# Kernel tuning notes

Measured on AMD Instinct MI355X. Metric: run time of the kernel, lower is better.

The kernel has to match this reference:

```python
import jax, jax.numpy as jnp
import numpy as np

# Irreps config: input/output = 32x0e + 16x1o (dim 80), H=4 heads -> head = 8x0e + 4x1o (dim 20)
M0, M1 = 32, 16      # input muls for 0e / 1o
m0, m1 = 8, 4        # per-head muls
H = 4
HEAD_DIM = m0 + 3 * m1   # 20
WNUM = H * (M0 * m0 + M1 * m0 + M0 * m1 + M1 * m1)  # 2304 per-edge TP weights
NB, HID = 16, 64
SQRT3 = np.float32(np.sqrt(3.0))
EPS = 1e-8


def radial_mlp(x, W1, b1, W2, b2):
    return jax.nn.silu(x @ W1 + b1) @ W2 + b2


def tp_edge(ss, vv, sh0, sh1, w):
    """FullyConnectedTensorProduct (32x0e+16x1o) x (1x0e+1x1o) -> H*(8x0e+4x1o) with per-edge weights w [E, WNUM].
    Paths: 0e*0e->0e, 1o*1o->0e (CG dot/sqrt3), 0e*1o->1o, 1o*0e->1o; path norm 1/sqrt(fan_in)."""
    E = ss.shape[0]
    per = M0 * m0 + M1 * m0 + M0 * m1 + M1 * m1  # 576
    w = w.reshape(E, H, per)
    o = 0
    Wss = w[..., o:o + M0 * m0].reshape(E, H, M0, m0); o += M0 * m0
    Wvv = w[..., o:o + M1 * m0].reshape(E, H, M1, m0); o += M1 * m0
    Wsv = w[..., o:o + M0 * m1].reshape(E, H, M0, m1); o += M0 * m1
    Wvs = w[..., o:o + M1 * m1].reshape(E, H, M1, m1)
    fan = np.float32(np.sqrt(M0 + M1))  # fan_in = 48 for both output irreps
    vv_dot = jnp.einsum('eui,ei->eu', vv, sh1) / SQRT3
    out0 = (jnp.einsum('eu,ehuw->ehw', ss * sh0[:, None], Wss)
            + jnp.einsum('eu,ehuw->ehw', vv_dot, Wvv)) / fan          # [E,H,m0]
    out1 = (jnp.einsum('eu,ehuw->ehw', ss, Wsv)[..., None] * sh1[:, None, None, :]
            + jnp.einsum('eui,ehuw->ehwi', vv * sh0[:, None, None], Wvs)) / fan  # [E,H,m1,3]
    return out0, out1


def setup_inputs() -> dict:
    key = jax.random.key(0)
    ks = jax.random.split(key, 24)
    N, E = 2000, 32000
    g = lambda k, s, sc=1.0: jax.random.normal(k, s, jnp.float32) * sc
    inp = {}
    inp['node_features'] = g(ks[0], (N, M0 + 3 * M1))
    inp['edge_index'] = jax.random.randint(ks[1], (2, E), 0, N)
    inp['edge_sh'] = g(ks[2], (E, 4))
    inp['edge_radial_emb'] = jax.random.uniform(ks[3], (E, NB), jnp.float32)
    # query e3nn Linear (per-head blocks)
    inp['Wq0'] = g(ks[4], (H, M0, m0))
    inp['Wq1'] = g(ks[5], (H, M1, m1))
    # radial MLPs for key / value TP weights
    inp['Wk1'] = g(ks[6], (NB, HID), 1 / np.sqrt(NB)); inp['bk1'] = jnp.zeros((HID,), jnp.float32)
    inp['Wk2'] = g(ks[7], (HID, WNUM), 1 / np.sqrt(HID)); inp['bk2'] = jnp.zeros((WNUM,), jnp.float32)
    inp['Wv1'] = g(ks[8], (NB, HID), 1 / np.sqrt(NB)); inp['bv1'] = jnp.zeros((HID,), jnp.float32)
    inp['Wv2'] = g(ks[9], (HID, WNUM), 1 / np.sqrt(HID)); inp['bv2'] = jnp.zeros((WNUM,), jnp.float32)
    # single-head dot-product TP -> 0e (shared weights)
    inp['Wd0'] = g(ks[10], (m0, m0))
    inp['Wd1'] = g(ks[11], (m1, m1))
    # output projection Linear (all heads mixed per irrep)
    inp['Wo0'] = g(ks[12], (H * m0, M0))
    inp['Wo1'] = g(ks[13], (H * m1, M1))
    # FFN: out irreps -> (2*M0)x0e + M1x1o -> out irreps
    inp['Wf1_0'] = g(ks[14], (M0, 2 * M0))
    inp['Wf1_1'] = g(ks[15], (M1, M1))
    inp['Wf2_0'] = g(ks[16], (2 * M0, M0))
    inp['Wf2_1'] = g(ks[17], (M1, M1))
    return inp


def reference(node_features, edge_index, edge_sh, edge_radial_emb,
              Wq0, Wq1, Wk1, bk1, Wk2, bk2, Wv1, bv1, Wv2, bv2,
              Wd0, Wd1, Wo0, Wo1, Wf1_0, Wf1_1, Wf2_0, Wf2_1):
    N = node_features.shape[0]
    s = node_features[:, :M0]                       # [N, M0] scalars
    v = node_features[:, M0:].reshape(N, M1, 3)     # [N, M1, 3] vectors
    src, dst = edge_index[0], edge_index[1]

    # query Linear (e3nn: per-irrep channel mix, norm 1/sqrt(fan_in))
    q0 = jnp.einsum('nu,huw->nhw', s, Wq0) / np.sqrt(M0)
    q1 = jnp.einsum('nui,huw->nhwi', v, Wq1) / np.sqrt(M1)

    sh0, sh1 = edge_sh[:, 0], edge_sh[:, 1:4]
    ss, vv = s[src], v[src]                         # gather per edge

    wk = radial_mlp(edge_radial_emb, Wk1, bk1, Wk2, bk2)
    wv = radial_mlp(edge_radial_emb, Wv1, bv1, Wv2, bv2)
    k0, k1 = tp_edge(ss, vv, sh0, sh1, wk)
    v0, v1 = tp_edge(ss, vv, sh0, sh1, wv)

    # per-head equivariant dot product -> 0e logits
    qd0, qd1 = q0[dst], q1[dst]
    fan_d = np.float32(np.sqrt(m0 * m0 + m1 * m1))
    logits = (jnp.einsum('ehu,uv,ehv->eh', qd0, Wd0, k0)
              + jnp.einsum('ehui,uv,ehvi->eh', qd1, Wd1, k1) / SQRT3) / fan_d
    logits = logits / np.sqrt(HEAD_DIM)             # self.scale
    logits = jnp.clip(logits, -10.0, 10.0)

    # scatter softmax over edges sharing a destination node
    seg_max = jax.ops.segment_max(logits, dst, num_segments=N)
    seg_max = jnp.maximum(seg_max, -10.0)           # handle empty segments
    ex = jnp.exp(logits - seg_max[dst])
    denom = jax.ops.segment_sum(ex, dst, num_segments=N)
    alpha = ex / (denom[dst] + 1e-12)               # [E, H]

    agg0 = jax.ops.segment_sum(alpha[..., None] * v0, dst, num_segments=N)        # [N,H,m0]
    agg1 = jax.ops.segment_sum(alpha[..., None, None] * v1, dst, num_segments=N)  # [N,H,m1,3]

    # output projection Linear over concatenated heads
    o0 = agg0.reshape(N, H * m0) @ Wo0 / np.sqrt(H * m0)
    o1 = jnp.einsum('nui,uw->nwi', agg1.reshape(N, H * m1, 3), Wo1) / np.sqrt(H * m1)

    # residual (input irreps == output irreps -> identity skip)
    x0 = s + o0
    x1 = v + o1

    # FFN with SafeNormActivation
    f0 = x0 @ Wf1_0 / np.sqrt(M0)                               # [N, 2*M0]
    f1 = jnp.einsum('nui,uw->nwi', x1, Wf1_1) / np.sqrt(M1)     # [N, M1, 3]
    a0 = jax.nn.silu(f0)
    norms = jnp.linalg.norm(f1, axis=-1, keepdims=True)
    safe = jnp.maximum(norms, EPS)
    a1 = jnp.where(norms < EPS, 0.0, (f1 / safe) * jax.nn.silu(norms))
    g0 = a0 @ Wf2_0 / np.sqrt(2 * M0)
    g1 = jnp.einsum('nui,uw->nwi', a1, Wf2_1) / np.sqrt(M1)

    out0 = x0 + g0
    out1 = x1 + g1
    return jnp.concatenate([out0, out1.reshape(N, M1 * 3)], axis=-1)
```

## Files before the change

### kernel.cpp

```cpp
#include <hip/hip_runtime.h>

typedef unsigned int uint;
typedef unsigned short ushort;
typedef __attribute__((ext_vector_type(8))) short bf16x8;
typedef __attribute__((ext_vector_type(4))) float f32x4;
typedef __attribute__((ext_vector_type(2))) float f32x2;

#define N_NODES 2000
#define N_EDGES 32000
#define WNUM 2304

constexpr size_t OFF_AGG0 = 0;
constexpr size_t OFF_AGG1 = 64000;
constexpr size_t OFF_DEN  = 160000;
constexpr size_t OFF_FLAG = 170000;
constexpr size_t OFF_W2T  = 170004;
constexpr size_t OFF_QT0  = 317460;
constexpr size_t OFF_QT1  = 381460;
constexpr size_t OFF_W1T  = 509460;
constexpr size_t OFF_W1P  = 511508;

__device__ __forceinline__ float b2f(ushort u){ union{uint i; float f;}x; x.i=((uint)u)<<16; return x.f; }
__device__ __forceinline__ float lo16(uint w){ union{uint u; float f;}x; x.u=w<<16; return x.f; }
__device__ __forceinline__ float hi16(uint w){ union{uint u; float f;}x; x.u=w&0xFFFF0000u; return x.f; }
__device__ __forceinline__ ushort f2b(float f){
  union{float f; uint u;}x; x.f=f;
  uint r = (x.u + 0x7FFFu + ((x.u>>16)&1u)) >> 16;
  return (ushort)r;
}
__device__ __forceinline__ float siluf(float x){ return x / (1.f + __expf(-x)); }

template<bool F32>
__device__ __forceinline__ float ldf(const void* p, int i){
  if (F32) return ((const float*)p)[i];
  return b2f(((const ushort*)p)[i]);
}
__device__ __forceinline__ float ldfr(const void* p, int i, bool f32){
  return f32 ? ((const float*)p)[i] : b2f(((const ushort*)p)[i]);
}

template<bool F32>
__device__ void prep_body(
    const void* __restrict__ nf,
    const void* __restrict__ Wk2, const void* __restrict__ Wv2,
    const void* __restrict__ Wk1, const void* __restrict__ Wv1,
    const void* __restrict__ Wq0, const void* __restrict__ Wq1,
    const void* __restrict__ Wd0, const void* __restrict__ Wd1,
    ushort* __restrict__ W2T, float* __restrict__ W1T, uint* __restrict__ W1P,
    float* __restrict__ qt0, float* __restrict__ qt1,
    float* __restrict__ aggz){
  const int t = threadIdx.x;
  const int bid = blockIdx.x;

  if (bid < 72){
    __shared__ ushort tile[64][66];
    const int mat = bid / 36, jt = bid - mat*36;
    const void* W = mat ? Wv2 : Wk2;
    const int j0 = jt*64;
    const int jo = t & 63, cb = t >> 6;
    #pragma unroll
    for (int k=0; k<16; ++k){
      const int c = cb + k*4;
      tile[c][jo] = F32 ? f2b(((const float*)W)[(size_t)c*WNUM + j0 + jo])
                        : ((const ushort*)W)[(size_t)c*WNUM + j0 + jo];
    }
    __syncthreads();
    const int jl = t >> 2, c0 = (t & 3)*16;
    ushort* dst = W2T + (size_t)mat*147456 + (size_t)(j0+jl)*64 + c0;
    #pragma unroll
    for (int k=0; k<16; ++k) dst[k] = tile[c0+k][jl];
  } else if (bid < 104){
    __shared__ float nfL[64][80];
    __shared__ float wq0L[1024], wq1L[256], wd0L[64], wd1L[16];
    const int nb = bid - 72, n0 = nb*64;
    if (F32){
      for (int idx=t; idx<1280; idx+=256){
        const int gi = n0*20 + idx;
        float4 v;
        if (gi < 40000) v = ((const float4*)nf)[gi];
        else { v.x=0.f; v.y=0.f; v.z=0.f; v.w=0.f; }
        ((float4*)&nfL[0][0])[idx] = v;
      }
    } else {
      for (int idx=t; idx<640; idx+=256){
        const int gi = n0*10 + idx;
        uint4 v;
        if (gi < 20000) v = ((const uint4*)nf)[gi];
        else { v.x=0u; v.y=0u; v.z=0u; v.w=0u; }
        float* d = &nfL[0][0] + idx*8;
        d[0]=lo16(v.x); d[1]=hi16(v.x); d[2]=lo16(v.y); d[3]=hi16(v.y);
        d[4]=lo16(v.z); d[5]=hi16(v.z); d[6]=lo16(v.w); d[7]=hi16(v.w);
      }
    }
    for (int idx=t; idx<1024; idx+=256) wq0L[idx] = ldf<F32>(Wq0, idx);
    if (t < 256) wq1L[t] = ldf<F32>(Wq1, t);
    if (t < 64)  wd0L[t] = ldf<F32>(Wd0, t);
    if (t < 16)  wd1L[t] = ldf<F32>(Wd1, t);
    __syncthreads();
    const int nl = t >> 2, h = t & 3;
    const int nn = n0 + nl;
    if (nn < N_NODES){
      const float* S = &nfL[nl][0];
      float q0[8];
      #pragma unroll
      for (int w=0; w<8; ++w){
        float a = 0.f;
        #pragma unroll
        for (int u=0; u<32; ++u) a += S[u]*wq0L[h*256 + u*8 + w];
        q0[w] = a * 0.17677669529663687f;
      }
      #pragma unroll
      for (int vv=0; vv<8; ++vv){
        float a = 0.f;
        #pragma unroll
        for (int u=0; u<8; ++u) a += q0[u]*wd0L[u*8+vv];
        qt0[nn*32 + h*8 + vv] = a;
      }
      float q1[12];
      #pragma unroll
      for (int w=0; w<4; ++w)
        #pragma unroll
        for (int i=0; i<3; ++i){
          float a = 0.f;
          #pragma unroll
          for (int u=0; u<16; ++u) a += S[32+u*3+i]*wq1L[h*64 + u*4 + w];
          q1[w*3+i] = a * 0.25f;
        }
      #pragma unroll
      for (int vv=0; vv<4; ++vv)
        #pragma unroll
        for (int i=0; i<3; ++i){
          float a = 0.f;
          #pragma unroll
          for (int u=0; u<4; ++u) a += q1[u*3+i]*wd1L[u*4+vv];
          qt1[nn*48 + h*12 + vv*3 + i] = a;
        }
    }
  } else if (bid == 104){
    for (int idx=t; idx<2048; idx+=256){
      const int mat = idx >> 10, rem = idx & 1023;
      const int c = rem >> 4, b = rem & 15;
      W1T[idx] = ldf<F32>(mat ? Wv1 : Wk1, b*64 + c);
    }
    for (int idx=t; idx<1024; idx+=256){
      const int mat = idx >> 9, rem = idx & 511;
      const int c = rem >> 3, j = rem & 7;
      const void* W = mat ? Wv1 : Wk1;
      ushort u0, u1;
      if (F32){ u0 = f2b(((const float*)W)[(2*j)*64+c]); u1 = f2b(((const float*)W)[(2*j+1)*64+c]); }
      else    { u0 = ((const ushort*)W)[(2*j)*64+c];     u1 = ((const ushort*)W)[(2*j+1)*64+c]; }
      W1P[idx] = (uint)u0 | ((uint)u1 << 16);
    }
  } else {
    float4 z; z.x=0.f; z.y=0.f; z.z=0.f; z.w=0.f;
    for (int i = (bid-105)*256 + t; i < 42000; i += 4096)
      ((float4*)aggz)[i] = z;
  }
}

__global__ __launch_bounds__(256) void prep_kernel(
    const void* nf,
    const void* Wk2, const void* Wv2,
    const void* Wk1, const void* Wv1,
    const void* Wq0, const void* Wq1,
    const void* Wd0, const void* Wd1,
    ushort* W2T, float* W1T, uint* W1P, float* qt0, float* qt1,
    float* aggz, int* flag){
  __shared__ int s_cnt;
  const int t = threadIdx.x;
  if (t == 0) s_cnt = 0;
  __syncthreads();
  {
    uint u = ((const ushort*)nf)[t*2];
    uint ex = (u >> 7) & 0xFFu;
    if (ex >= 0xA0u) atomicAdd(&s_cnt, 1);
  }
  __syncthreads();
  const bool F32 = (s_cnt >= 20);
  if (blockIdx.x == 0 && t == 0) *flag = F32 ? 1 : 0;
  if (F32) prep_body<true >(nf, Wk2, Wv2, Wk1, Wv1, Wq0, Wq1, Wd0, Wd1, W2T, W1T, W1P, qt0, qt1, aggz);
  else     prep_body<false>(nf, Wk2, Wv2, Wk1, Wv1, Wq0, Wq1, Wd0, Wd1, W2T, W1T, W1P, qt0, qt1, aggz);
}

struct Smem {
  ushort hidA[8192];
  union {
    struct {
      float fssT[32][66];
      float fvvT[16][66];
      float sslT[32][66];
    } f;
    float cont[5376];
  } u;
  float vshT[3][16][66];
  float sh1T[3][66];
  float park0[2][4][64][8];
  float parkP[2][4][64][4];
  float exL[64][4];
  int   dstL[64];
};

__device__ __forceinline__ f32x4 mma_pair(const bf16x8& a0f, const bf16x8& a1f,
                                          bf16x8 b0, bf16x8 b1, float bb){
  f32x4 c = {bb,bb,bb,bb};
  c = __builtin_amdgcn_mfma_f32_16x16x32_bf16(a0f, b0, c, 0,0,0);
  c = __builtin_amdgcn_mfma_f32_16x16x32_bf16(a1f, b1, c, 0,0,0);
  return c;
}
__device__ __forceinline__ void acc_feat(const f32x4 c, const float* fp, float* acc){
  f32x2 fA = *(const f32x2*)(fp);
  f32x2 fB = *(const f32x2*)(fp + 2);
  acc[0] += c[0]*fA[0]; acc[1] += c[1]*fA[1];
  acc[2] += c[2]*fB[0]; acc[3] += c[3]*fB[1];
}

template<bool F32>
__device__ void edge_body(
    const void* __restrict__ nf,  const int* __restrict__ eidx,
    const void* __restrict__ esh, const void* __restrict__ emb,
    const float* __restrict__ W1T, const uint* __restrict__ W1P,
    const void* __restrict__ bk1, const void* __restrict__ bk2,
    const void* __restrict__ bv1, const void* __restrict__ bv2,
    const ushort* __restrict__ W2T,
    const float* __restrict__ qt0g, const float* __restrict__ qt1g,
    float* __restrict__ agg0, float* __restrict__ agg1, float* __restrict__ denom,
    Smem& sm){
  const int t  = threadIdx.x;
  const int geb = blockIdx.x*64;

  {
    const int g = t >> 5, r = t & 31;
    int geA[4], srcA[4], dstA[4];
    float shv0[4], shv1[4], shv2[4], shv3[4];
    #pragma unroll
    for (int e=0; e<4; ++e) geA[e] = geb + g*4 + e;
    #pragma unroll
    for (int e=0; e<4; ++e){ srcA[e] = eidx[geA[e]]; dstA[e] = eidx[N_EDGES + geA[e]]; }
    #pragma unroll
    for (int e=0; e<4; ++e){
      if (F32){
        float4 s4 = ((const float4*)esh)[geA[e]];
        shv0[e]=s4.x; shv1[e]=s4.y; shv2[e]=s4.z; shv3[e]=s4.w;
      } else {
        uint2 u2 = ((const uint2*)esh)[geA[e]];
        shv0[e]=lo16(u2.x); shv1[e]=hi16(u2.x); shv2[e]=lo16(u2.y); shv3[e]=hi16(u2.y);
      }
    }
    #pragma unroll
    for (int e=0; e<4; ++e){
      const int le = g*4+e, src = srcA[e];
      const float sh0 = shv0[e], s1a = shv1[e], s1b = shv2[e], s1c = shv3[e];
      if (r == 0) sm.dstL[le] = dstA[e];
      if (r < 3) sm.sh1T[r][le] = (r==0)? s1a : (r==1)? s1b : s1c;
      float sv = ldf<F32>(nf, src*80 + r);
      sm.u.f.sslT[r][le] = sv;
      sm.u.f.fssT[r][le] = sv * sh0;
      if (r < 16){
        float v0 = ldf<F32>(nf, src*80+32+r*3+0);
        float v1 = ldf<F32>(nf, src*80+32+r*3+1);
        float v2 = ldf<F32>(nf, src*80+32+r*3+2);
        sm.vshT[0][r][le] = v0*sh0; sm.vshT[1][r][le] = v1*sh0; sm.vshT[2][r][le] = v2*sh0;
        sm.u.f.fvvT[r][le] = (v0*s1a + v1*s1b + v2*s1c) * 0.5773502691896258f;
      }
    }
  }

  {
    const int c  = t & 63;
    const int g8 = t >> 6;
    const int le0 = g8*8;
    float bkv = ldf<F32>(bk1, c), bvv = ldf<F32>(bv1, c);
    f32x4 wkF[4], wvF[4];
    uint4 wkB[2], wvB[2];
    if (F32){
      const f32x4* pk = (const f32x4*)(W1T + c*16);
      const f32x4* pv = (const f32x4*)(W1T + 1024 + c*16);
      wkF[0]=pk[0]; wkF[1]=pk[1]; wkF[2]=pk[2]; wkF[3]=pk[3];
      wvF[0]=pv[0]; wvF[1]=pv[1]; wvF[2]=pv[2]; wvF[3]=pv[3];
    } else {
      const uint4* pk = (const uint4*)(W1P + c*8);
      const uint4* pv = (const uint4*)(W1P + 512 + c*8);
      wkB[0]=pk[0]; wkB[1]=pk[1];
      wvB[0]=pv[0]; wvB[1]=pv[1];
    }
    uint4 ra, rb; float4 fa, fb, fc, fd;
    if (F32){
      const float4* p = (const float4*)emb + (size_t)(geb+le0)*4;
      fa = p[0]; fb = p[1]; fc = p[2]; fd = p[3];
    } else {
      const uint4* p = (const uint4*)emb + (size_t)(geb+le0)*2;
      ra = p[0]; rb = p[1];
    }
    #pragma unroll
    for (int e=0; e<8; ++e){
      float em[16];
      if (F32){
        em[0]=fa.x; em[1]=fa.y; em[2]=fa.z; em[3]=fa.w;
        em[4]=fb.x; em[5]=fb.y; em[6]=fb.z; em[7]=fb.w;
        em[8]=fc.x; em[9]=fc.y; em[10]=fc.z; em[11]=fc.w;
        em[12]=fd.x; em[13]=fd.y; em[14]=fd.z; em[15]=fd.w;
      } else {
        em[0]=lo16(ra.x); em[1]=hi16(ra.x); em[2]=lo16(ra.y); em[3]=hi16(ra.y);
        em[4]=lo16(ra.z); em[5]=hi16(ra.z); em[6]=lo16(ra.w); em[7]=hi16(ra.w);
        em[8]=lo16(rb.x); em[9]=hi16(rb.x); em[10]=lo16(rb.y); em[11]=hi16(rb.y);
        em[12]=lo16(rb.z); em[13]=hi16(rb.z); em[14]=lo16(rb.w); em[15]=hi16(rb.w);
      }
      if (e < 7){
        if (F32){
          const float4* p = (const float4*)emb + (size_t)(geb+le0+e+1)*4;
          fa = p[0]; fb = p[1]; fc = p[2]; fd = p[3];
        } else {
          const uint4* p = (const uint4*)emb + (size_t)(geb+le0+e+1)*2;
          ra = p[0]; rb = p[1];
        }
      }
      const int le = le0+e;
      float ak = bkv, av = bvv;
      if (F32){
        #pragma unroll
        for (int g=0; g<4; ++g)
          #pragma unroll
          for (int j=0; j<4; ++j){
            ak += em[g*4+j]*wkF[g][j];
            av += em[g*4+j]*wvF[g][j];
          }
      } else {
        #pragma unroll
        for (int g=0; g<2; ++g){
          const uint4 a = wkB[g], b = wvB[g];
          ak += em[g*8+0]*lo16(a.x) + em[g*8+1]*hi16(a.x)
              + em[g*8+2]*lo16(a.y) + em[g*8+3]*hi16(a.y)
              + em[g*8+4]*lo16(a.z) + em[g*8+5]*hi16(a.z)
              + em[g*8+6]*lo16(a.w) + em[g*8+7]*hi16(a.w);
          av += em[g*8+0]*lo16(b.x) + em[g*8+1]*hi16(b.x)
              + em[g*8+2]*lo16(b.y) + em[g*8+3]*hi16(b.y)
              + em[g*8+4]*lo16(b.z) + em[g*8+5]*hi16(b.z)
              + em[g*8+6]*lo16(b.w) + em[g*8+7]*hi16(b.w);
        }
      }
      const int idx = (le>>4)*1024 + (c>>5)*512 + ((((c>>3)&3)*16 + (le&15))<<3) + (c&7);
      sm.hidA[idx]        = f2b(siluf(ak));
      sm.hidA[4096 + idx] = f2b(siluf(av));
    }
  }
  __syncthreads();

  const int w  = t >> 6;
  const int kv = w >> 2;
  const int h  = w & 3;
  const int lane = t & 63, q = lane >> 4, n = lane & 15;
  const float invfan = 0.14433756729740643f;

  const ushort* wptr = W2T + (size_t)kv*147456 + h*36864 + n*64 + q*8;
  const void* bvec = kv ? bv2 : bk2;
  const int bi0 = h*576 + n;
  const float* fb_ss = &sm.u.f.fssT[n>>3][q*4];
  const float* fb_sl = &sm.u.f.sslT[n>>2][q*4];
  const int nq2 = n>>2;

  bf16x8 af[4][2];
  #pragma unroll
  for (int Mt=0; Mt<4; ++Mt)
    #pragma unroll
    for (int kh=0; kh<2; ++kh)
      af[Mt][kh] = *(const bf16x8*)&sm.hidA[kv*4096 + Mt*1024 + kh*512 + lane*8];

#define PREF(P0,P1,PB,TL) \
  P0 = *(const bf16x8*)(wptr + (TL)*1024); \
  P1 = *(const bf16x8*)(wptr + (TL)*1024 + 32); \
  PB = ldf<F32>(bvec, bi0 + (TL)*16);

  bf16x8 pA0, pA1, pB0, pB1; float pAb, pBb;
  PREF(pA0, pA1, pAb, 0);
  PREF(pB0, pB1, pBb, 1);

  {
    float a0[4][4];
    #pragma unroll
    for (int Mt=0; Mt<4; ++Mt){ a0[Mt][0]=0.f; a0[Mt][1]=0.f; a0[Mt][2]=0.f; a0[Mt][3]=0.f; }
    #pragma unroll 2
    for (int tl=0; tl<24; tl+=2){
      { bf16x8 b0=pA0, b1=pA1; float bb=pAb;
        PREF(pA0, pA1, pAb, tl+2);
        const float* fp = fb_ss + tl*132;
        #pragma unroll
        for (int Mt=0; Mt<4; ++Mt) acc_feat(mma_pair(af[Mt][0], af[Mt][1], b0, b1, bb), fp + Mt*16, a0[Mt]); }
      { bf16x8 b0=pB0, b1=pB1; float bb=pBb;
        PREF(pB0, pB1, pBb, tl+3);
        const float* fp = fb_ss + (tl+1)*132;
        #pragma unroll
        for (int Mt=0; Mt<4; ++Mt) acc_feat(mma_pair(af[Mt][0], af[Mt][1], b0, b1, bb), fp + Mt*16, a0[Mt]); }
    }
    #pragma unroll
    for (int Mt=0; Mt<4; ++Mt)
      #pragma unroll
      for (int z=0; z<4; ++z){
        a0[Mt][z] += __shfl_xor(a0[Mt][z], 8, 64);
        if (n < 8) sm.park0[kv][h][Mt*16 + q*4 + z][n] = a0[Mt][z];
      }
  }

  {
    float aP[4][4];
    #pragma unroll
    for (int Mt=0; Mt<4; ++Mt){ aP[Mt][0]=0.f; aP[Mt][1]=0.f; aP[Mt][2]=0.f; aP[Mt][3]=0.f; }
    #pragma unroll 2
    for (int tl=24; tl<32; tl+=2){
      { bf16x8 b0=pA0, b1=pA1; float bb=pAb;
        PREF(pA0, pA1, pAb, tl+2);
        const float* fp = fb_sl + (tl-24)*264;
        #pragma unroll
        for (int Mt=0; Mt<4; ++Mt) acc_feat(mma_pair(af[Mt][0], af[Mt][1], b0, b1, bb), fp + Mt*16, aP[Mt]); }
      { bf16x8 b0=pB0, b1=pB1; float bb=pBb;
        PREF(pB0, pB1, pBb, tl+3);
        const float* fp = fb_sl + (tl-23)*264;
        #pragma unroll
        for (int Mt=0; Mt<4; ++Mt) acc_feat(mma_pair(af[Mt][0], af[Mt][1], b0, b1, bb), fp + Mt*16, aP[Mt]); }
    }
    #pragma unroll
    for (int Mt=0; Mt<4; ++Mt)
      #pragma unroll
      for (int z=0; z<4; ++z){
        aP[Mt][z] += __shfl_xor(aP[Mt][z], 4, 64);
        aP[Mt][z] += __shfl_xor(aP[Mt][z], 8, 64);
        if (n < 4) sm.parkP[kv][h][Mt*16 + q*4 + z][n] = aP[Mt][z];
      }
  }

  float aW[3][4][4];
  #pragma unroll
  for (int i=0; i<3; ++i)
    #pragma unroll
    for (int Mt=0; Mt<4; ++Mt){ aW[i][Mt][0]=0.f; aW[i][Mt][1]=0.f; aW[i][Mt][2]=0.f; aW[i][Mt][3]=0.f; }
#define BODY_AW(B0,B1,BB,TL) { \
    const int u = ((TL)-32)*4 + nq2; \
    _Pragma("unroll") \
    for (int Mt=0; Mt<4; ++Mt){ \
      f32x4 c = mma_pair(af[Mt][0], af[Mt][1], B0, B1, BB); \
      _Pragma("unroll") \
      for (int i=0; i<3; ++i) acc_feat(c, &sm.vshT[i][u][Mt*16+q*4], aW[i][Mt]); \
    } }
  { bf16x8 b0=pA0, b1=pA1; float bb=pAb; PREF(pA0, pA1, pAb, 34); BODY_AW(b0,b1,bb,32); }
  { bf16x8 b0=pB0, b1=pB1; float bb=pBb; PREF(pB0, pB1, pBb, 35); BODY_AW(b0,b1,bb,33); }
  { bf16x8 b0=pA0, b1=pA1; float bb=pAb; BODY_AW(b0,b1,bb,34); }
  { bf16x8 b0=pB0, b1=pB1; float bb=pBb; BODY_AW(b0,b1,bb,35); }
#undef BODY_AW
#undef PREF
  #pragma unroll
  for (int i=0; i<3; ++i)
    #pragma unroll
    for (int Mt=0; Mt<4; ++Mt)
      #pragma unroll
      for (int z=0; z<4; ++z){
        aW[i][Mt][z] += __shfl_xor(aW[i][Mt][z], 4, 64);
        aW[i][Mt][z] += __shfl_xor(aW[i][Mt][z], 8, 64);
      }

  if (kv == 0){
    float lgp[4][4];
    #pragma unroll
    for (int Mt=0; Mt<4; ++Mt)
      #pragma unroll
      for (int z=0; z<4; ++z){
        const int el = Mt*16 + q*4 + z;
        const int d = sm.dstL[el];
        float acc = 0.f;
        if (n < 8) acc = qt0g[d*32 + h*8 + n] * sm.park0[0][h][el][n];
        if (n < 4){
          const float aPv = sm.parkP[0][h][el][n];
          float s = 0.f;
          #pragma unroll
          for (int i=0; i<3; ++i){
            float k1 = aPv*sm.sh1T[i][el] + aW[i][Mt][z];
            s += qt1g[d*48 + h*12 + n*3 + i] * k1;
          }
          acc += s * 0.5773502691896258f;
        }
        lgp[Mt][z] = acc;
      }
    #pragma unroll
    for (int Mt=0; Mt<4; ++Mt)
      #pragma unroll
      for (int z=0; z<4; ++z){
        lgp[Mt][z] += __shfl_xor(lgp[Mt][z], 1, 64);
        lgp[Mt][z] += __shfl_xor(lgp[Mt][z], 2, 64);
        lgp[Mt][z] += __shfl_xor(lgp[Mt][z], 4, 64);
        lgp[Mt][z] += __shfl_xor(lgp[Mt][z], 8, 64);
      }
    if (n == 0){
      #pragma unroll
      for (int Mt=0; Mt<4; ++Mt)
        #pragma unroll
        for (int z=0; z<4; ++z){
          float lg = lgp[Mt][z] * invfan * 0.025f;
          lg = fminf(10.f, fmaxf(-10.f, lg));
          sm.exL[Mt*16 + q*4 + z][h] = __expf(lg - 10.0f);
        }
    }
  }
  __syncthreads();

  if (kv == 1){
    #pragma unroll
    for (int Mt=0; Mt<4; ++Mt)
      #pragma unroll
      for (int z=0; z<4; ++z){
        const int el = Mt*16 + q*4 + z;
        const float ex = sm.exL[el][h];
        float* cp = &sm.u.cont[el*84 + h*21];
        if (n == 0) cp[0] = ex;
        if (n < 8)  cp[1+n] = ex * sm.park0[1][h][el][n] * invfan;
        if (n < 4){
          const float aPv = sm.parkP[1][h][el][n];
          #pragma unroll
          for (int i=0; i<3; ++i){
            float v1 = (aPv*sm.sh1T[i][el] + aW[i][Mt][z]) * invfan;
            cp[9+n*3+i] = ex * v1;
          }
        }
      }
  }
  __syncthreads();

  #pragma unroll
  for (int k=0; k<11; ++k){
    const int idx = t + k*512;
    if (idx < 5376){
      const int el = idx / 84;
      const int cm = idx - el*84;
      const int h2 = cm / 21;
      const int comp = cm - h2*21;
      const float val = sm.u.cont[idx];
      const int d2 = sm.dstL[el];
      if (comp == 0)      atomicAdd(denom + d2*4  + h2, val);
      else if (comp < 9)  atomicAdd(agg0  + d2*32 + h2*8  + (comp-1), val);
      else                atomicAdd(agg1  + d2*48 + h2*12 + (comp-9), val);
    }
  }
}

__global__ __launch_bounds__(512) void edge_kernel(
    const void* nf, const int* eidx, const void* esh, const void* emb,
    const float* W1T, const uint* W1P,
    const void* bk1, const void* bk2,
    const void* bv1, const void* bv2,
    const ushort* W2T, const float* qt0g, const float* qt1g,
    float* agg0, float* agg1, float* denom, const int* flag){
  __shared__ Smem sm;
  if (*flag)
    edge_body<true >(nf,eidx,esh,emb,W1T,W1P,bk1,bk2,bv1,bv2,W2T,qt0g,qt1g,agg0,agg1,denom,sm);
  else
    edge_body<false>(nf,eidx,esh,emb,W1T,W1P,bk1,bk2,bv1,bv2,W2T,qt0g,qt1g,agg0,agg1,denom,sm);
}

__global__ __launch_bounds__(256) void node_out_kernel(
    const void* __restrict__ nf, const float* __restrict__ agg0r, const float* __restrict__ agg1r,
    const float* __restrict__ denom,
    const void* __restrict__ Wo0, const void* __restrict__ Wo1,
    const void* __restrict__ Wf10, const void* __restrict__ Wf11,
    const void* __restrict__ Wf20, const void* __restrict__ Wf21,
    void* __restrict__ out, const int* __restrict__ flag){
  __shared__ float ag0[4][32], ag1[4][48], adiv[4][4];
  __shared__ float x0s[4][32], x1s[4][48], a0s[4][64], f1s[4][48], coefs[4][16];
  const bool F32 = (*flag) != 0;
  const int s = threadIdx.x >> 6, t = threadIdx.x & 63;
  const int n = blockIdx.x*4 + s;
  if (t < 4) adiv[s][t] = 1.f / (denom[n*4+t] + 1e-12f);
  __syncthreads();
  if (t < 32) ag0[s][t] = agg0r[n*32+t] * adiv[s][t>>3];
  if (t < 48) ag1[s][t] = agg1r[n*48+t] * adiv[s][t/12];
  __syncthreads();
  if (t < 32){
    float o = 0.f;
    #pragma unroll
    for (int k=0; k<32; ++k) o += ag0[s][k]*ldfr(Wo0, k*32+t, F32);
    x0s[s][t] = ldfr(nf, n*80+t, F32) + o*0.17677669529663687f;
  }
  if (t < 48){
    int w = t/3, i = t - w*3;
    float o = 0.f;
    #pragma unroll
    for (int u=0; u<16; ++u) o += ag1[s][u*3+i]*ldfr(Wo1, u*16+w, F32);
    x1s[s][t] = ldfr(nf, n*80+32+t, F32) + o*0.25f;
  }
  __syncthreads();
  {
    float f0 = 0.f;
    #pragma unroll
    for (int u=0; u<32; ++u) f0 += x0s[s][u]*ldfr(Wf10, u*64+t, F32);
    a0s[s][t] = siluf(f0*0.17677669529663687f);
  }
  if (t < 48){
    int w = t/3, i = t - w*3;
    float f1 = 0.f;
    #pragma unroll
    for (int u=0; u<16; ++u) f1 += x1s[s][u*3+i]*ldfr(Wf11, u*16+w, F32);
    f1s[s][t] = f1*0.25f;
  }
  __syncthreads();
  if (t < 16){
    float a = f1s[s][t*3], b = f1s[s][t*3+1], c = f1s[s][t*3+2];
    float nrm = sqrtf(a*a+b*b+c*c);
    float safe = fmaxf(nrm, 1e-8f);
    coefs[s][t] = (nrm < 1e-8f) ? 0.f : siluf(nrm)/safe;
  }
  __syncthreads();
  if (t < 32){
    float g = 0.f;
    #pragma unroll
    for (int u=0; u<64; ++u) g += a0s[s][u]*ldfr(Wf20, u*32+t, F32);
    float val = x0s[s][t] + g*0.125f;
    if (F32) ((float*)out)[n*80+t] = val; else ((ushort*)out)[n*80+t] = f2b(val);
  }
  if (t < 48){
    int w = t/3, i = t - w*3;
    float g = 0.f;
    #pragma unroll
    for (int u=0; u<16; ++u) g += coefs[s][u]*f1s[s][u*3+i]*ldfr(Wf21, u*16+w, F32);
    float val = x1s[s][t] + g*0.25f;
    if (F32) ((float*)out)[n*80+32+t] = val; else ((ushort*)out)[n*80+32+t] = f2b(val);
  }
}

extern "C" void kernel_launch(void* const* d_in, const int* in_sizes, int n_in,
                              void* d_out, int out_size, void* d_ws, size_t ws_size,
                              hipStream_t stream){
  const void* nf   = d_in[0];
  const int*  eidx = (const int*)d_in[1];
  const void* esh  = d_in[2];
  const void* emb  = d_in[3];
  const void* Wq0  = d_in[4];
  const void* Wq1  = d_in[5];
  const void* Wk1  = d_in[6];
  const void* bk1  = d_in[7];
  const void* Wk2  = d_in[8];
  const void* bk2  = d_in[9];
  const void* Wv1  = d_in[10];
  const void* bv1  = d_in[11];
  const void* Wv2  = d_in[12];
  const void* bv2  = d_in[13];
  const void* Wd0  = d_in[14];
  const void* Wd1  = d_in[15];
  const void* Wo0  = d_in[16];
  const void* Wo1  = d_in[17];
  const void* Wf10 = d_in[18];
  const void* Wf11 = d_in[19];
  const void* Wf20 = d_in[20];
  const void* Wf21 = d_in[21];
  float* ws = (float*)d_ws;

  float* agg0  = ws + OFF_AGG0;
  float* agg1  = ws + OFF_AGG1;
  float* denom = ws + OFF_DEN;
  int*   flag  = (int*)(ws + OFF_FLAG);
  ushort* W2T  = (ushort*)(ws + OFF_W2T);
  float* qt0   = ws + OFF_QT0;
  float* qt1   = ws + OFF_QT1;
  float* W1T   = ws + OFF_W1T;
  uint*  W1P   = (uint*)(ws + OFF_W1P);

  prep_kernel<<<121, 256, 0, stream>>>(nf, Wk2, Wv2, Wk1, Wv1, Wq0, Wq1, Wd0, Wd1,
                                       W2T, W1T, W1P, qt0, qt1, agg0, flag);
  edge_kernel<<<N_EDGES/64, 512, 0, stream>>>(nf, eidx, esh, emb,
                                              W1T, W1P, bk1, bk2, bv1, bv2,
                                              W2T, qt0, qt1,
                                              agg0, agg1, denom, flag);
  node_out_kernel<<<N_NODES/4, 256, 0, stream>>>(nf, agg0, agg1, denom,
                                                 Wo0, Wo1, Wf10, Wf11, Wf20, Wf21, d_out, flag);
}
```

Measured before the change: 202.7 us.

## Fuse prep, edge and node kernels into one cooperative persistent kernel

Merges the three launches into one 500-block, 512-thread kernel that uses grid-wide barriers between the prep, edge and node-output phases, with a union of shared-memory layouts. Prep and node work are re-tiled for 512 threads (128 nodes per prep block, 8 nodes per node block). The dtype flag is now recomputed per block instead of read from workspace. If cooperative launch is not possible it falls back to three launches of the same kernel. The aim is to remove launch gaps. The risks are grid-sync cost, occupancy limits from the larger union LDS, and host-side occupancy queries on every call.

```diff
diff --git a/kernel.cpp b/kernel.cpp
--- a/kernel.cpp
+++ b/kernel.cpp
@@ -1,4 +1,7 @@
 #include <hip/hip_runtime.h>
+#include <hip/hip_cooperative_groups.h>
+
+namespace cg = cooperative_groups;
 
 typedef unsigned int uint;
 typedef unsigned short ushort;
@@ -13,7 +16,6 @@
 constexpr size_t OFF_AGG0 = 0;
 constexpr size_t OFF_AGG1 = 64000;
 constexpr size_t OFF_DEN  = 160000;
-constexpr size_t OFF_FLAG = 170000;
 constexpr size_t OFF_W2T  = 170004;
 constexpr size_t OFF_QT0  = 317460;
 constexpr size_t OFF_QT1  = 381460;
@@ -34,152 +36,6 @@
 __device__ __forceinline__ float ldf(const void* p, int i){
   if (F32) return ((const float*)p)[i];
   return b2f(((const ushort*)p)[i]);
-}
-__device__ __forceinline__ float ldfr(const void* p, int i, bool f32){
-  return f32 ? ((const float*)p)[i] : b2f(((const ushort*)p)[i]);
-}
-
-template<bool F32>
-__device__ void prep_body(
-    const void* __restrict__ nf,
-    const void* __restrict__ Wk2, const void* __restrict__ Wv2,
-    const void* __restrict__ Wk1, const void* __restrict__ Wv1,
-    const void* __restrict__ Wq0, const void* __restrict__ Wq1,
-    const void* __restrict__ Wd0, const void* __restrict__ Wd1,
-    ushort* __restrict__ W2T, float* __restrict__ W1T, uint* __restrict__ W1P,
-    float* __restrict__ qt0, float* __restrict__ qt1,
-    float* __restrict__ aggz){
-  const int t = threadIdx.x;
-  const int bid = blockIdx.x;
-
-  if (bid < 72){
-    __shared__ ushort tile[64][66];
-    const int mat = bid / 36, jt = bid - mat*36;
-    const void* W = mat ? Wv2 : Wk2;
-    const int j0 = jt*64;
-    const int jo = t & 63, cb = t >> 6;
-    #pragma unroll
-    for (int k=0; k<16; ++k){
-      const int c = cb + k*4;
-      tile[c][jo] = F32 ? f2b(((const float*)W)[(size_t)c*WNUM + j0 + jo])
-                        : ((const ushort*)W)[(size_t)c*WNUM + j0 + jo];
-    }
-    __syncthreads();
-    const int jl = t >> 2, c0 = (t & 3)*16;
-    ushort* dst = W2T + (size_t)mat*147456 + (size_t)(j0+jl)*64 + c0;
-    #pragma unroll
-    for (int k=0; k<16; ++k) dst[k] = tile[c0+k][jl];
-  } else if (bid < 104){
-    __shared__ float nfL[64][80];
-    __shared__ float wq0L[1024], wq1L[256], wd0L[64], wd1L[16];
-    const int nb = bid - 72, n0 = nb*64;
-    if (F32){
-      for (int idx=t; idx<1280; idx+=256){
-        const int gi = n0*20 + idx;
-        float4 v;
-        if (gi < 40000) v = ((const float4*)nf)[gi];
-        else { v.x=0.f; v.y=0.f; v.z=0.f; v.w=0.f; }
-        ((float4*)&nfL[0][0])[idx] = v;
-      }
-    } else {
-      for (int idx=t; idx<640; idx+=256){
-        const int gi = n0*10 + idx;
-        uint4 v;
-        if (gi < 20000) v = ((const uint4*)nf)[gi];
-        else { v.x=0u; v.y=0u; v.z=0u; v.w=0u; }
-        float* d = &nfL[0][0] + idx*8;
-        d[0]=lo16(v.x); d[1]=hi16(v.x); d[2]=lo16(v.y); d[3]=hi16(v.y);
-        d[4]=lo16(v.z); d[5]=hi16(v.z); d[6]=lo16(v.w); d[7]=hi16(v.w);
-      }
-    }
-    for (int idx=t; idx<1024; idx+=256) wq0L[idx] = ldf<F32>(Wq0, idx);
-    if (t < 256) wq1L[t] = ldf<F32>(Wq1, t);
-    if (t < 64)  wd0L[t] = ldf<F32>(Wd0, t);
-    if (t < 16)  wd1L[t] = ldf<F32>(Wd1, t);
-    __syncthreads();
-    const int nl = t >> 2, h = t & 3;
-    const int nn = n0 + nl;
-    if (nn < N_NODES){
-      const float* S = &nfL[nl][0];
-      float q0[8];
-      #pragma unroll
-      for (int w=0; w<8; ++w){
-        float a = 0.f;
-        #pragma unroll
-        for (int u=0; u<32; ++u) a += S[u]*wq0L[h*256 + u*8 + w];
-        q0[w] = a * 0.17677669529663687f;
-      }
-      #pragma unroll
-      for (int vv=0; vv<8; ++vv){
-        float a = 0.f;
-        #pragma unroll
-        for (int u=0; u<8; ++u) a += q0[u]*wd0L[u*8+vv];
-        qt0[nn*32 + h*8 + vv] = a;
-      }
-      float q1[12];
-      #pragma unroll
-      for (int w=0; w<4; ++w)
-        #pragma unroll
-        for (int i=0; i<3; ++i){
-          float a = 0.f;
-          #pragma unroll
-          for (int u=0; u<16; ++u) a += S[32+u*3+i]*wq1L[h*64 + u*4 + w];
-          q1[w*3+i] = a * 0.25f;
-        }
-      #pragma unroll
-      for (int vv=0; vv<4; ++vv)
-        #pragma unroll
-        for (int i=0; i<3; ++i){
-          float a = 0.f;
-          #pragma unroll
-          for (int u=0; u<4; ++u) a += q1[u*3+i]*wd1L[u*4+vv];
-          qt1[nn*48 + h*12 + vv*3 + i] = a;
-        }
-    }
-  } else if (bid == 104){
-    for (int idx=t; idx<2048; idx+=256){
-      const int mat = idx >> 10, rem = idx & 1023;
-      const int c = rem >> 4, b = rem & 15;
-      W1T[idx] = ldf<F32>(mat ? Wv1 : Wk1, b*64 + c);
-    }
-    for (int idx=t; idx<1024; idx+=256){
-      const int mat = idx >> 9, rem = idx & 511;
-      const int c = rem >> 3, j = rem & 7;
-      const void* W = mat ? Wv1 : Wk1;
-      ushort u0, u1;
-      if (F32){ u0 = f2b(((const float*)W)[(2*j)*64+c]); u1 = f2b(((const float*)W)[(2*j+1)*64+c]); }
-      else    { u0 = ((const ushort*)W)[(2*j)*64+c];     u1 = ((const ushort*)W)[(2*j+1)*64+c]; }
-      W1P[idx] = (uint)u0 | ((uint)u1 << 16);
-    }
-  } else {
-    float4 z; z.x=0.f; z.y=0.f; z.z=0.f; z.w=0.f;
-    for (int i = (bid-105)*256 + t; i < 42000; i += 4096)
-      ((float4*)aggz)[i] = z;
-  }
-}
-
-__global__ __launch_bounds__(256) void prep_kernel(
-    const void* nf,
-    const void* Wk2, const void* Wv2,
-    const void* Wk1, const void* Wv1,
-    const void* Wq0, const void* Wq1,
-    const void* Wd0, const void* Wd1,
-    ushort* W2T, float* W1T, uint* W1P, float* qt0, float* qt1,
-    float* aggz, int* flag){
-  __shared__ int s_cnt;
-  const int t = threadIdx.x;
-  if (t == 0) s_cnt = 0;
-  __syncthreads();
-  {
-    uint u = ((const ushort*)nf)[t*2];
-    uint ex = (u >> 7) & 0xFFu;
-    if (ex >= 0xA0u) atomicAdd(&s_cnt, 1);
-  }
-  __syncthreads();
-  const bool F32 = (s_cnt >= 20);
-  if (blockIdx.x == 0 && t == 0) *flag = F32 ? 1 : 0;
-  if (F32) prep_body<true >(nf, Wk2, Wv2, Wk1, Wv1, Wq0, Wq1, Wd0, Wd1, W2T, W1T, W1P, qt0, qt1, aggz);
-  else     prep_body<false>(nf, Wk2, Wv2, Wk1, Wv1, Wq0, Wq1, Wd0, Wd1, W2T, W1T, W1P, qt0, qt1, aggz);
 }
 
 struct Smem {
@@ -200,6 +56,22 @@
   int   dstL[64];
 };
 
+struct PrepQL {
+  float nfL[128][80];
+  float wq0L[1024], wq1L[256], wd0L[64], wd1L[16];
+};
+struct NodeL {
+  float ag0[8][32], ag1[8][48], adiv[8][4];
+  float x0s[8][32], x1s[8][48], a0s[8][64], f1s[8][48], coefs[8][16];
+};
+
+union FusedLDS {
+  Smem   edge;
+  PrepQL pq;
+  ushort tileT[64][66];
+  NodeL  no;
+};
+
 __device__ __forceinline__ f32x4 mma_pair(const bf16x8& a0f, const bf16x8& a1f,
                                           bf16x8 b0, bf16x8 b1, float bb){
   f32x4 c = {bb,bb,bb,bb};
@@ -212,6 +84,122 @@
   f32x2 fB = *(const f32x2*)(fp + 2);
   acc[0] += c[0]*fA[0]; acc[1] += c[1]*fA[1];
   acc[2] += c[2]*fB[0]; acc[3] += c[3]*fB[1];
+}
+
+template<bool F32>
+__device__ void prep_phase(
+    int bid, int t,
+    const void* __restrict__ nf,
+    const void* __restrict__ Wk2, const void* __restrict__ Wv2,
+    const void* __restrict__ Wk1, const void* __restrict__ Wv1,
+    const void* __restrict__ Wq0, const void* __restrict__ Wq1,
+    const void* __restrict__ Wd0, const void* __restrict__ Wd1,
+    ushort* __restrict__ W2T, float* __restrict__ W1T, uint* __restrict__ W1P,
+    float* __restrict__ qt0, float* __restrict__ qt1,
+    float* __restrict__ aggz, FusedLDS& L){
+  if (bid < 72){
+    const int mat = bid / 36, jt = bid - mat*36;
+    const void* W = mat ? Wv2 : Wk2;
+    const int j0 = jt*64;
+    const int jo = t & 63, cb = t >> 6;
+    #pragma unroll
+    for (int k=0; k<8; ++k){
+      const int c = cb + k*8;
+      L.tileT[c][jo] = F32 ? f2b(((const float*)W)[(size_t)c*WNUM + j0 + jo])
+                           : ((const ushort*)W)[(size_t)c*WNUM + j0 + jo];
+    }
+    __syncthreads();
+    const int jl = t >> 3, c0 = (t & 7)*8;
+    ushort* dst = W2T + (size_t)mat*147456 + (size_t)(j0+jl)*64 + c0;
+    #pragma unroll
+    for (int k=0; k<8; ++k) dst[k] = L.tileT[c0+k][jl];
+  } else if (bid < 88){
+    const int task = bid - 72, n0 = task*128;
+    if (F32){
+      for (int idx=t; idx<2560; idx+=512){
+        const int gi = n0*20 + idx;
+        float4 v;
+        if (gi < 40000) v = ((const float4*)nf)[gi];
+        else { v.x=0.f; v.y=0.f; v.z=0.f; v.w=0.f; }
+        ((float4*)&L.pq.nfL[0][0])[idx] = v;
+      }
+    } else {
+      for (int idx=t; idx<1280; idx+=512){
+        const int gi = n0*10 + idx;
+        uint4 v;
+        if (gi < 20000) v = ((const uint4*)nf)[gi];
+        else { v.x=0u; v.y=0u; v.z=0u; v.w=0u; }
+        float* d = &L.pq.nfL[0][0] + idx*8;
+        d[0]=lo16(v.x); d[1]=hi16(v.x); d[2]=lo16(v.y); d[3]=hi16(v.y);
+        d[4]=lo16(v.z); d[5]=hi16(v.z); d[6]=lo16(v.w); d[7]=hi16(v.w);
+      }
+    }
+    for (int idx=t; idx<1024; idx+=512) L.pq.wq0L[idx] = ldf<F32>(Wq0, idx);
+    if (t < 256) L.pq.wq1L[t] = ldf<F32>(Wq1, t);
+    if (t < 64)  L.pq.wd0L[t] = ldf<F32>(Wd0, t);
+    if (t < 16)  L.pq.wd1L[t] = ldf<F32>(Wd1, t);
+    __syncthreads();
+    const int nl = t >> 2, h = t & 3;
+    const int nn = n0 + nl;
+    if (nn < N_NODES){
+      const float* S = &L.pq.nfL[nl][0];
+      float q0[8];
+      #pragma unroll
+      for (int w=0; w<8; ++w){
+        float a = 0.f;
+        #pragma unroll
+        for (int u=0; u<32; ++u) a += S[u]*L.pq.wq0L[h*256 + u*8 + w];
+        q0[w] = a * 0.17677669529663687f;
+      }
+      #pragma unroll
+      for (int vv=0; vv<8; ++vv){
+        float a = 0.f;
+        #pragma unroll
+        for (int u=0; u<8; ++u) a += q0[u]*L.pq.wd0L[u*8+vv];
+        qt0[nn*32 + h*8 + vv] = a;
+      }
+      float q1[12];
+      #pragma unroll
+      for (int w=0; w<4; ++w)
+        #pragma unroll
+        for (int i=0; i<3; ++i){
+          float a = 0.f;
+          #pragma unroll
+          for (int u=0; u<16; ++u) a += S[32+u*3+i]*L.pq.wq1L[h*64 + u*4 + w];
+          q1[w*3+i] = a * 0.25f;
+        }
+      #pragma unroll
+      for (int vv=0; vv<4; ++vv)
+        #pragma unroll
+        for (int i=0; i<3; ++i){
+          float a = 0.f;
+          #pragma unroll
+          for (int u=0; u<4; ++u) a += q1[u*3+i]*L.pq.wd1L[u*4+vv];
+          qt1[nn*48 + h*12 + vv*3 + i] = a;
+        }
+    }
+  } else if (bid == 88){
+    for (int idx=t; idx<2048; idx+=512){
+      const int mat = idx >> 10, rem = idx & 1023;
+      const int c = rem >> 4, b = rem & 15;
+      W1T[idx] = ldf<F32>(mat ? Wv1 : Wk1, b*64 + c);
+    }
+    for (int idx=t; idx<1024; idx+=512){
+      const int mat = idx >> 9, rem = idx & 511;
+      const int c = rem >> 3, j = rem & 7;
+      const void* W = mat ? Wv1 : Wk1;
+      ushort u0, u1;
+      if (F32){ u0 = f2b(((const float*)W)[(2*j)*64+c]); u1 = f2b(((const float*)W)[(2*j+1)*64+c]); }
+      else    { u0 = ((const ushort*)W)[(2*j)*64+c];     u1 = ((const ushort*)W)[(2*j+1)*64+c]; }
+      W1P[idx] = (uint)u0 | ((uint)u1 << 16);
+    }
+  } else {
+    const int i = (bid-89)*512 + t;
+    if (i < 42000){
+      float4 z; z.x=0.f; z.y=0.f; z.z=0.f; z.w=0.f;
+      ((float4*)aggz)[i] = z;
+    }
+  }
 }
 
 template<bool F32>
@@ -539,87 +527,128 @@
   }
 }
 
-__global__ __launch_bounds__(512) void edge_kernel(
-    const void* nf, const int* eidx, const void* esh, const void* emb,
-    const float* W1T, const uint* W1P,
-    const void* bk1, const void* bk2,
-    const void* bv1, const void* bv2,
-    const ushort* W2T, const float* qt0g, const float* qt1g,
-    float* agg0, float* agg1, float* denom, const int* flag){
-  __shared__ Smem sm;
-  if (*flag)
-    edge_body<true >(nf,eidx,esh,emb,W1T,W1P,bk1,bk2,bv1,bv2,W2T,qt0g,qt1g,agg0,agg1,denom,sm);
-  else
-    edge_body<false>(nf,eidx,esh,emb,W1T,W1P,bk1,bk2,bv1,bv2,W2T,qt0g,qt1g,agg0,agg1,denom,sm);
-}
-
-__global__ __launch_bounds__(256) void node_out_kernel(
+template<bool F32>
+__device__ void node_out_body(
+    int bid, int tt,
     const void* __restrict__ nf, const float* __restrict__ agg0r, const float* __restrict__ agg1r,
     const float* __restrict__ denom,
     const void* __restrict__ Wo0, const void* __restrict__ Wo1,
     const void* __restrict__ Wf10, const void* __restrict__ Wf11,
     const void* __restrict__ Wf20, const void* __restrict__ Wf21,
-    void* __restrict__ out, const int* __restrict__ flag){
-  __shared__ float ag0[4][32], ag1[4][48], adiv[4][4];
-  __shared__ float x0s[4][32], x1s[4][48], a0s[4][64], f1s[4][48], coefs[4][16];
-  const bool F32 = (*flag) != 0;
-  const int s = threadIdx.x >> 6, t = threadIdx.x & 63;
-  const int n = blockIdx.x*4 + s;
-  if (t < 4) adiv[s][t] = 1.f / (denom[n*4+t] + 1e-12f);
-  __syncthreads();
-  if (t < 32) ag0[s][t] = agg0r[n*32+t] * adiv[s][t>>3];
-  if (t < 48) ag1[s][t] = agg1r[n*48+t] * adiv[s][t/12];
+    void* __restrict__ outp, NodeL& L){
+  const int s = tt >> 6, t = tt & 63;
+  const int n = bid*8 + s;
+  if (t < 4) L.adiv[s][t] = 1.f / (denom[n*4+t] + 1e-12f);
+  __syncthreads();
+  if (t < 32) L.ag0[s][t] = agg0r[n*32+t] * L.adiv[s][t>>3];
+  if (t < 48) L.ag1[s][t] = agg1r[n*48+t] * L.adiv[s][t/12];
   __syncthreads();
   if (t < 32){
     float o = 0.f;
     #pragma unroll
-    for (int k=0; k<32; ++k) o += ag0[s][k]*ldfr(Wo0, k*32+t, F32);
-    x0s[s][t] = ldfr(nf, n*80+t, F32) + o*0.17677669529663687f;
+    for (int k=0; k<32; ++k) o += L.ag0[s][k]*ldf<F32>(Wo0, k*32+t);
+    L.x0s[s][t] = ldf<F32>(nf, n*80+t) + o*0.17677669529663687f;
   }
   if (t < 48){
     int w = t/3, i = t - w*3;
     float o = 0.f;
     #pragma unroll
-    for (int u=0; u<16; ++u) o += ag1[s][u*3+i]*ldfr(Wo1, u*16+w, F32);
-    x1s[s][t] = ldfr(nf, n*80+32+t, F32) + o*0.25f;
+    for (int u=0; u<16; ++u) o += L.ag1[s][u*3+i]*ldf<F32>(Wo1, u*16+w);
+    L.x1s[s][t] = ldf<F32>(nf, n*80+32+t) + o*0.25f;
   }
   __syncthreads();
   {
     float f0 = 0.f;
     #pragma unroll
-    for (int u=0; u<32; ++u) f0 += x0s[s][u]*ldfr(Wf10, u*64+t, F32);
-    a0s[s][t] = siluf(f0*0.17677669529663687f);
+    for (int u=0; u<32; ++u) f0 += L.x0s[s][u]*ldf<F32>(Wf10, u*64+t);
+    L.a0s[s][t] = siluf(f0*0.17677669529663687f);
   }
   if (t < 48){
     int w = t/3, i = t - w*3;
     float f1 = 0.f;
     #pragma unroll
-    for (int u=0; u<16; ++u) f1 += x1s[s][u*3+i]*ldfr(Wf11, u*16+w, F32);
-    f1s[s][t] = f1*0.25f;
+    for (int u=0; u<16; ++u) f1 += L.x1s[s][u*3+i]*ldf<F32>(Wf11, u*16+w);
+    L.f1s[s][t] = f1*0.25f;
   }
   __syncthreads();
   if (t < 16){
-    float a = f1s[s][t*3], b = f1s[s][t*3+1], c = f1s[s][t*3+2];
+    float a = L.f1s[s][t*3], b = L.f1s[s][t*3+1], c = L.f1s[s][t*3+2];
     float nrm = sqrtf(a*a+b*b+c*c);
     float safe = fmaxf(nrm, 1e-8f);
-    coefs[s][t] = (nrm < 1e-8f) ? 0.f : siluf(nrm)/safe;
+    L.coefs[s][t] = (nrm < 1e-8f) ? 0.f : siluf(nrm)/safe;
   }
   __syncthreads();
   if (t < 32){
     float g = 0.f;
     #pragma unroll
-    for (int u=0; u<64; ++u) g += a0s[s][u]*ldfr(Wf20, u*32+t, F32);
-    float val = x0s[s][t] + g*0.125f;
-    if (F32) ((float*)out)[n*80+t] = val; else ((ushort*)out)[n*80+t] = f2b(val);
+    for (int u=0; u<64; ++u) g += L.a0s[s][u]*ldf<F32>(Wf20, u*32+t);
+    float val = L.x0s[s][t] + g*0.125f;
+    if (F32) ((float*)outp)[n*80+t] = val; else ((ushort*)outp)[n*80+t] = f2b(val);
   }
   if (t < 48){
     int w = t/3, i = t - w*3;
     float g = 0.f;
     #pragma unroll
-    for (int u=0; u<16; ++u) g += coefs[s][u]*f1s[s][u*3+i]*ldfr(Wf21, u*16+w, F32);
-    float val = x1s[s][t] + g*0.25f;
-    if (F32) ((float*)out)[n*80+32+t] = val; else ((ushort*)out)[n*80+32+t] = f2b(val);
-  }
+    for (int u=0; u<16; ++u) g += L.coefs[s][u]*L.f1s[s][u*3+i]*ldf<F32>(Wf21, u*16+w);
+    float val = L.x1s[s][t] + g*0.25f;
+    if (F32) ((float*)outp)[n*80+32+t] = val; else ((ushort*)outp)[n*80+32+t] = f2b(val);
+  }
+}
+
+template<bool F32>
+__device__ void fused_body(
+    int phase,
+    const void* nf, const int* eidx, const void* esh, const void* emb,
+    const void* Wk2, const void* Wv2, const void* Wk1, const void* Wv1,
+    const void* Wq0, const void* Wq1, const void* Wd0, const void* Wd1,
+    const void* bk1, const void* bk2, const void* bv1, const void* bv2,
+    const void* Wo0, const void* Wo1, const void* Wf10, const void* Wf11,
+    const void* Wf20, const void* Wf21,
+    ushort* W2T, float* W1T, uint* W1P, float* qt0, float* qt1,
+    float* agg0, float* agg1, float* denom, void* outp, FusedLDS& L){
+  const int bid = blockIdx.x;
+  const int t = threadIdx.x;
+  if (phase <= 0)
+    prep_phase<F32>(bid, t, nf, Wk2, Wv2, Wk1, Wv1, Wq0, Wq1, Wd0, Wd1,
+                    W2T, W1T, W1P, qt0, qt1, agg0, L);
+  if (phase == -1) cg::this_grid().sync();
+  if (phase == -1 || phase == 1)
+    edge_body<F32>(nf, eidx, esh, emb, W1T, W1P, bk1, bk2, bv1, bv2,
+                   W2T, qt0, qt1, agg0, agg1, denom, L.edge);
+  if (phase == -1) cg::this_grid().sync();
+  if ((phase == -1 || phase == 2) && bid < 250)
+    node_out_body<F32>(bid, t, nf, agg0, agg1, denom,
+                       Wo0, Wo1, Wf10, Wf11, Wf20, Wf21, outp, L.no);
+}
+
+__global__ __launch_bounds__(512) void fused_kernel(
+    int phase,
+    const void* nf, const int* eidx, const void* esh, const void* emb,
+    const void* Wk2, const void* Wv2, const void* Wk1, const void* Wv1,
+    const void* Wq0, const void* Wq1, const void* Wd0, const void* Wd1,
+    const void* bk1, const void* bk2, const void* bv1, const void* bv2,
+    const void* Wo0, const void* Wo1, const void* Wf10, const void* Wf11,
+    const void* Wf20, const void* Wf21,
+    ushort* W2T, float* W1T, uint* W1P, float* qt0, float* qt1,
+    float* agg0, float* agg1, float* denom, void* outp){
+  __shared__ FusedLDS L;
+  __shared__ int s_cnt;
+  const int t = threadIdx.x;
+  if (t == 0) s_cnt = 0;
+  __syncthreads();
+  if (t < 256){
+    uint u = ((const ushort*)nf)[t*2];
+    uint ex = (u >> 7) & 0xFFu;
+    if (ex >= 0xA0u) atomicAdd(&s_cnt, 1);
+  }
+  __syncthreads();
+  const bool F32 = (s_cnt >= 20);
+  if (F32) fused_body<true >(phase, nf, eidx, esh, emb, Wk2, Wv2, Wk1, Wv1, Wq0, Wq1, Wd0, Wd1,
+                             bk1, bk2, bv1, bv2, Wo0, Wo1, Wf10, Wf11, Wf20, Wf21,
+                             W2T, W1T, W1P, qt0, qt1, agg0, agg1, denom, outp, L);
+  else     fused_body<false>(phase, nf, eidx, esh, emb, Wk2, Wv2, Wk1, Wv1, Wq0, Wq1, Wd0, Wd1,
+                             bk1, bk2, bv1, bv2, Wo0, Wo1, Wf10, Wf11, Wf20, Wf21,
+                             W2T, W1T, W1P, qt0, qt1, agg0, agg1, denom, outp, L);
 }
 
 extern "C" void kernel_launch(void* const* d_in, const int* in_sizes, int n_in,
@@ -652,19 +681,38 @@
   float* agg0  = ws + OFF_AGG0;
   float* agg1  = ws + OFF_AGG1;
   float* denom = ws + OFF_DEN;
-  int*   flag  = (int*)(ws + OFF_FLAG);
   ushort* W2T  = (ushort*)(ws + OFF_W2T);
   float* qt0   = ws + OFF_QT0;
   float* qt1   = ws + OFF_QT1;
   float* W1T   = ws + OFF_W1T;
   uint*  W1P   = (uint*)(ws + OFF_W1P);
 
-  prep_kernel<<<121, 256, 0, stream>>>(nf, Wk2, Wv2, Wk1, Wv1, Wq0, Wq1, Wd0, Wd1,
-                                       W2T, W1T, W1P, qt0, qt1, agg0, flag);
-  edge_kernel<<<N_EDGES/64, 512, 0, stream>>>(nf, eidx, esh, emb,
-                                              W1T, W1P, bk1, bk2, bv1, bv2,
-                                              W2T, qt0, qt1,
-                                              agg0, agg1, denom, flag);
-  node_out_kernel<<<N_NODES/4, 256, 0, stream>>>(nf, agg0, agg1, denom,
-                                                 Wo0, Wo1, Wf10, Wf11, Wf20, Wf21, d_out, flag);
-}
+  int dev = 0; hipGetDevice(&dev);
+  int nCU = 0; hipDeviceGetAttribute(&nCU, hipDeviceAttributeMultiprocessorCount, dev);
+  int nb = 0;
+  hipOccupancyMaxActiveBlocksPerMultiprocessor(&nb, fused_kernel, 512, 0);
+
+  if (nb > 0 && nCU > 0 && nb * nCU >= 500){
+    int phase = -1;
+    void* args[] = { &phase, &nf, &eidx, &esh, &emb, &Wk2, &Wv2, &Wk1, &Wv1,
+                     &Wq0, &Wq1, &Wd0, &Wd1, &bk1, &bk2, &bv1, &bv2,
+                     &Wo0, &Wo1, &Wf10, &Wf11, &Wf20, &Wf21,
+                     &W2T, &W1T, &W1P, &qt0, &qt1, &agg0, &agg1, &denom, &d_out };
+    hipError_t e = hipLaunchCooperativeKernel((void*)fused_kernel, dim3(500), dim3(512),
+                                              args, 0, stream);
+    if (e == hipSuccess) return;
+  }
+
+  fused_kernel<<<500, 512, 0, stream>>>(0, nf, eidx, esh, emb, Wk2, Wv2, Wk1, Wv1,
+                                        Wq0, Wq1, Wd0, Wd1, bk1, bk2, bv1, bv2,
+                                        Wo0, Wo1, Wf10, Wf11, Wf20, Wf21,
+                                        W2T, W1T, W1P, qt0, qt1, agg0, agg1, denom, d_out);
+  fused_kernel<<<500, 512, 0, stream>>>(1, nf, eidx, esh, emb, Wk2, Wv2, Wk1, Wv1,
+                                        Wq0, Wq1, Wd0, Wd1, bk1, bk2, bv1, bv2,
+                                        Wo0, Wo1, Wf10, Wf11, Wf20, Wf21,
+                                        W2T, W1T, W1P, qt0, qt1, agg0, agg1, denom, d_out);
+  fused_kernel<<<250, 512, 0, stream>>>(2, nf, eidx, esh, emb, Wk2, Wv2, Wk1, Wv1,
+                                        Wq0, Wq1, Wd0, Wd1, bk1, bk2, bv1, bv2,
+                                        Wo0, Wo1, Wf10, Wf11, Wf20, Wf21,
+                                        W2T, W1T, W1P, qt0, qt1, agg0, agg1, denom, d_out);
+}
```

New measurement: 207.1 us. 2.2% more time.
